# Performance work log

Measured on AMD Instinct MI355X. Metric: run time of the kernel, lower is better.

The kernel has to match this reference:

```python
import jax, jax.numpy as jnp
import numpy as np

B, S, D, H, DK, R = 8, 1024, 1024, 8, 128, 16
NEG = float(-2**31)


def setup_inputs() -> dict:
    key = jax.random.key(0)
    ks = jax.random.split(key, 16)
    std = 1.0 / np.sqrt(D)
    inp = {
        "query": jax.random.normal(ks[0], (B, S, D), jnp.float32),
        "key": jax.random.normal(ks[1], (B, S, D), jnp.float32),
        "value": jax.random.normal(ks[2], (B, S, D), jnp.float32),
        "mask": jax.random.bernoulli(ks[3], 0.9, (B, S, S)),
        "W_A": jax.random.normal(ks[4], (D, R), jnp.float32) * std,
        "W_B": jax.random.normal(ks[5], (R, H * DK), jnp.float32) * std,
        "W_C": jax.random.normal(ks[6], (D, R), jnp.float32) * std,
        "W_D": jax.random.normal(ks[7], (R, H * DK), jnp.float32) * std,
        "W_E": jax.random.normal(ks[8], (D, R), jnp.float32) * std,
        "W_F": jax.random.normal(ks[9], (R, H * DK), jnp.float32) * std,
        "Wq": jax.random.normal(ks[10], (D, H * DK), jnp.float32) * std,
        "bq": jnp.zeros((H * DK,), jnp.float32),
        "Wk": jax.random.normal(ks[11], (D, H * DK), jnp.float32) * std,
        "bk": jnp.zeros((H * DK,), jnp.float32),
        "Wv": jax.random.normal(ks[12], (D, H * DK), jnp.float32) * std,
        "bv": jnp.zeros((H * DK,), jnp.float32),
        "Wo": jax.random.normal(ks[13], (H * DK, D), jnp.float32) * std,
        "bo": jnp.zeros((D,), jnp.float32),
    }
    return inp


def reference(query, key, value, mask, W_A, W_B, W_C, W_D, W_E, W_F,
              Wq, bq, Wk, bk, Wv, bv, Wo, bo):
    nb = query.shape[0]
    # Linear + low-rank (LoRA-style) add; low-rank applied right-to-left for efficiency
    q = query @ Wq + bq + (query @ W_A) @ W_B      # [B,S,H*DK]
    k = key @ Wk + bk + (key @ W_C) @ W_D
    v = value @ Wv + bv + (value @ W_E) @ W_F
    # faithful plain reshape (NOT a transpose), as in the original code
    q = q.reshape(nb, H, -1, DK)                   # [B,H,S,DK]
    k = k.reshape(nb, H, -1, DK)
    v = v.reshape(nb, H, -1, DK)
    m = mask[:, None, :, :]                        # [B,1,S,S] broadcasts over heads
    scores = jnp.einsum("bhqd,bhkd->bhqk", q, k)   # no 1/sqrt(dk) scaling (faithful)
    scores = jnp.where(m, scores, jnp.float32(NEG))
    p = jax.nn.softmax(scores, axis=-1)
    x = jnp.einsum("bhqk,bhkd->bhqd", p, v)
    x = x.reshape(nb, -1, H * DK)                  # [B,S,H*DK]
    return x @ Wo + bo
```

## Files before the change

kernel.cpp:

```cpp
#include <hip/hip_runtime.h>
#include <hip/hip_bf16.h>
#include <stdint.h>


#define kB 8
#define kS 1024
#define kD 1024
#define kH 8
#define kDK 128
#define kHDK 1024
#define kM (kB * kS)
#define kMaskWords (kB * kS * (kS / 64))
#define kQKVN (kM * kHDK)

typedef _Float16 f16;
typedef __attribute__((ext_vector_type(4))) float f32x4;
typedef __attribute__((ext_vector_type(8))) _Float16 f16x8;

#define OFF_FLAG  ((size_t)0)
#define OFF_MBITS ((size_t)256)
#define OFF_WQT   (OFF_MBITS + (size_t)kMaskWords * 8)
#define OFF_WKT   (OFF_WQT + (size_t)2097152)
#define OFF_WVT   (OFF_WKT + (size_t)2097152)
#define OFF_WOT   (OFF_WVT + (size_t)2097152)
#define OFF_Q     (OFF_WOT + (size_t)2097152)
#define OFF_K     (OFF_Q  + (size_t)kQKVN * 2)
#define OFF_VT    (OFF_K  + (size_t)kQKVN * 2)
#define OFF_X     (OFF_VT + (size_t)kQKVN * 2)
#define OFF_T0    OFF_X
#define OFF_T1    (OFF_X + (size_t)kQKVN * 2)
#define OFF_T2    (OFF_X + (size_t)kQKVN * 4)
#define NEED3     (OFF_X + (size_t)kQKVN * 6)

__device__ __forceinline__ void async_load16(const void* g, void* lds_uniform) {
  auto gp = reinterpret_cast<const __attribute__((address_space(1))) unsigned int*>(
      reinterpret_cast<uintptr_t>(g));
  auto lp = reinterpret_cast<__attribute__((address_space(3))) unsigned int*>(
      reinterpret_cast<uintptr_t>(lds_uniform));
  __builtin_amdgcn_global_load_lds(gp, lp, 16, 0, 0);
}

__device__ __forceinline__ f32x4 mfma16(f16x8 a, f16x8 b, f32x4 c) {
  return __builtin_amdgcn_mfma_f32_16x16x32_f16(a, b, c, 0, 0, 0);
}

__device__ __forceinline__ float ldw(const void* p, size_t i, int f) {
  return f ? ((const float*)p)[i] : (float)((const __bf16*)p)[i];
}

__device__ __forceinline__ void swz_tiles(int& mt, int& nt) {
  const int gx = gridDim.x, gy = gridDim.y;
  const int L = blockIdx.y * gx + blockIdx.x;
  const int xcd = L & 7, rank = L >> 3;
  mt = xcd * (gy >> 3) + rank / gx;
  nt = rank % gx;
}

__global__ void detect_kernel(const unsigned int* __restrict__ qw,
                              const unsigned int* __restrict__ mw,
                              int* __restrict__ flags) {
  const int lane = threadIdx.x & 63;
  int hi = 0; bool w4 = true, b1 = true;
  #pragma unroll
  for (int j = 0; j < 4; ++j) {
    unsigned int w = qw[lane * 4 + j];
    hi += (int)(((w >> 7) & 0xFF) > 0x90) + (int)(((w >> 23) & 0xFF) > 0x90);
    unsigned int m = mw[lane * 4 + j];
    if (!(m == 0u || m == 1u || m == 0x3F800000u)) w4 = false;
    if ((m & 0xFEFEFEFEu) != 0u) b1 = false;
  }
  #pragma unroll
  for (int off = 32; off; off >>= 1) hi += __shfl_xor(hi, off, 64);
  unsigned long long bw4 = __ballot(w4), bb1 = __ballot(b1);
  if (lane == 0 && blockIdx.x == 0) {
    flags[1] = (hi > 16) ? 1 : 0;
    flags[0] = (bw4 == ~0ull) ? 4 : ((bb1 == ~0ull) ? 1 : 2);
  }
}

__global__ void pack_mask_kernel(const void* __restrict__ mask, const int* __restrict__ flags,
                                 unsigned long long* __restrict__ mbits) {
  int wi = blockIdx.x * 4 + (threadIdx.x >> 6);
  if (wi >= kMaskWords) return;
  int lane = threadIdx.x & 63;
  size_t e = (size_t)wi * 64 + lane;
  int width = flags[0];
  bool on;
  if (width == 1)      on = ((const unsigned char*)mask)[e] != 0;
  else if (width == 2) on = ((const unsigned short*)mask)[e] != 0;
  else                 on = ((const unsigned int*)mask)[e] != 0;
  unsigned long long bal = __ballot(on);
  if (lane == 0) mbits[wi] = bal;
}

__device__ __forceinline__ void convert_body(const void* src, f16* dst,
                                             const int* flags, int i) {
  f16x8 o;
  if (flags[1]) {
    f32x4 a = *(const f32x4*)((const float*)src + i);
    f32x4 b = *(const f32x4*)((const float*)src + i + 4);
    #pragma unroll
    for (int j = 0; j < 4; ++j) { o[j] = (f16)a[j]; o[4 + j] = (f16)b[j]; }
  } else {
    const __bf16* s = (const __bf16*)src + i;
    #pragma unroll
    for (int j = 0; j < 8; ++j) o[j] = (f16)(float)s[j];
  }
  *(f16x8*)(dst + i) = o;
}

__global__ __launch_bounds__(256) void convert_kernel(
    const void* __restrict__ src, f16* __restrict__ dst,
    const int* __restrict__ flags, int n) {
  const int i = (blockIdx.x * 256 + threadIdx.x) * 8;
  if (i < n) convert_body(src, dst, flags, i);
}

__global__ __launch_bounds__(256) void convert3_kernel(
    const void* __restrict__ s0, const void* __restrict__ s1, const void* __restrict__ s2,
    f16* __restrict__ d0, f16* __restrict__ d1, f16* __restrict__ d2,
    const int* __restrict__ flags) {
  const int z = blockIdx.z;
  const void* src = (z == 0) ? s0 : (z == 1) ? s1 : s2;
  f16* dst = (z == 0) ? d0 : (z == 1) ? d1 : d2;
  const int i = (blockIdx.x * 256 + threadIdx.x) * 8;
  if (i < kQKVN) convert_body(src, dst, flags, i);
}

__global__ __launch_bounds__(256) void build_weights_kernel(
    const void* __restrict__ Wq, const void* __restrict__ WA, const void* __restrict__ WB,
    const void* __restrict__ Wk, const void* __restrict__ WC, const void* __restrict__ WD,
    const void* __restrict__ Wv, const void* __restrict__ WE, const void* __restrict__ WF,
    const void* __restrict__ Wo, const int* __restrict__ flags,
    f16* __restrict__ WqT, f16* __restrict__ WkT,
    f16* __restrict__ WvT, f16* __restrict__ WoT) {
  const int z = blockIdx.z;
  const int f = flags[1];
  const void *W, *Aw = nullptr, *Bw = nullptr;
  f16* Out;
  if (z == 0)      { W = Wq; Aw = WA; Bw = WB; Out = WqT; }
  else if (z == 1) { W = Wk; Aw = WC; Bw = WD; Out = WkT; }
  else if (z == 2) { W = Wv; Aw = WE; Bw = WF; Out = WvT; }
  else             { W = Wo;                   Out = WoT; }

  __shared__ float Wt[32][33];
  __shared__ float At[32][16];
  __shared__ float Bt[16][33];
  const int tx = threadIdx.x, ty = threadIdx.y;
  const int k0 = blockIdx.y * 32, n0 = blockIdx.x * 32;
  #pragma unroll
  for (int i = 0; i < 4; ++i)
    Wt[ty + 8 * i][tx] = ldw(W, (size_t)(k0 + ty + 8 * i) * 1024 + n0 + tx, f);
  const int t = ty * 32 + tx;
  if (Aw) {
    #pragma unroll
    for (int j = 0; j < 2; ++j) {
      int e = t + j * 256;
      At[e >> 4][e & 15] = ldw(Aw, (size_t)(k0 + (e >> 4)) * 16 + (e & 15), f);
    }
    #pragma unroll
    for (int j = 0; j < 2; ++j) {
      int e = t + j * 256;
      Bt[e >> 5][e & 31] = ldw(Bw, (size_t)(e >> 5) * 1024 + n0 + (e & 31), f);
    }
  }
  __syncthreads();
  #pragma unroll
  for (int i = 0; i < 4; ++i) {
    const int nloc = ty + 8 * i, kloc = tx;
    float acc = Wt[kloc][nloc];
    if (Aw) {
      #pragma unroll
      for (int r = 0; r < 16; ++r) acc += At[kloc][r] * Bt[r][nloc];
    }
    Out[(size_t)(n0 + nloc) * 1024 + k0 + kloc] = (f16)acc;
  }
}

__device__ __forceinline__ void gemm_epilogue(
    f32x4 acc[4][4], const void* bias, void* C, int f, int vtrans, int out_dyn,
    int N, int m0, int n0, int wr, int wc, int l15, int hi) {
  const int wf32 = out_dyn && f;
  #pragma unroll
  for (int mi = 0; mi < 4; ++mi) {
    #pragma unroll
    for (int ni = 0; ni < 4; ++ni) {
      #pragma unroll
      for (int r = 0; r < 4; ++r) {
        const int row = m0 + wr * 64 + mi * 16 + 4 * hi + r;
        const int col = n0 + wc * 64 + ni * 16 + l15;
        float v = acc[mi][ni][r] + (bias ? ldw(bias, col, f) : 0.f);
        if (vtrans) {
          const int b = row >> 10, sp = row & 1023;
          const int fi = (sp << 10) | col;
          const int h = fi >> 17, s = (fi >> 7) & 1023, d = fi & 127;
          ((f16*)C)[(((size_t)(b * 8 + h) * 128 + d) << 10) + s] = (f16)v;
        } else if (wf32) {
          ((float*)C)[(size_t)row * N + col] = v;
        } else if (out_dyn) {
          ((__bf16*)C)[(size_t)row * N + col] = (__bf16)v;
        } else {
          ((f16*)C)[(size_t)row * N + col] = (f16)v;
        }
      }
    }
  }
}

__device__ __forceinline__ void gemm_core64(
    const f16* A, const f16* BT, const void* bias, void* C,
    int f, int vtrans, int out_dyn, int N, int K,
    int m0, int n0, f16* As, f16* Bs) {
  const int tid = threadIdx.x;
  const int lane = tid & 63, w = tid >> 6;
  const int wr = w >> 1, wc = w & 1;
  const int l15 = lane & 15, hi = lane >> 4;

  f32x4 acc[4][4];
  #pragma unroll
  for (int i = 0; i < 4; ++i)
    #pragma unroll
    for (int j = 0; j < 4; ++j) acc[i][j] = (f32x4){0.f, 0.f, 0.f, 0.f};

  for (int k0 = 0; k0 < K; k0 += 64) {
    if (k0) __syncthreads();
    #pragma unroll
    for (int j = 0; j < 4; ++j) {
      int d = tid + j * 256;
      int row = d >> 3, piece = (d & 7) ^ (row & 7);
      async_load16(A  + (size_t)(m0 + row) * K + k0 + piece * 8,
                   (char*)As + (w * 64 + j * 256) * 16);
      async_load16(BT + (size_t)(n0 + row) * K + k0 + piece * 8,
                   (char*)Bs + (w * 64 + j * 256) * 16);
    }
    __syncthreads();

    #pragma unroll
    for (int kk = 0; kk < 2; ++kk) {
      f16x8 af[4], bf_[4];
      #pragma unroll
      for (int mi = 0; mi < 4; ++mi) {
        const int row = wr * 64 + mi * 16 + l15;
        af[mi] = *(const f16x8*)&As[row * 64 + (((kk * 4 + hi) ^ (row & 7)) << 3)];
      }
      #pragma unroll
      for (int ni = 0; ni < 4; ++ni) {
        const int row = wc * 64 + ni * 16 + l15;
        bf_[ni] = *(const f16x8*)&Bs[row * 64 + (((kk * 4 + hi) ^ (row & 7)) << 3)];
      }
      #pragma unroll
      for (int mi = 0; mi < 4; ++mi)
        #pragma unroll
        for (int ni = 0; ni < 4; ++ni)
          acc[mi][ni] = mfma16(af[mi], bf_[ni], acc[mi][ni]);
    }
  }

  gemm_epilogue(acc, bias, C, f, vtrans, out_dyn, N, m0, n0, wr, wc, l15, hi);
}

__global__ __launch_bounds__(256) void gemm_bt_kernel(
    const f16* __restrict__ A, const f16* __restrict__ BT,
    const void* __restrict__ bias, void* __restrict__ C,
    const int* __restrict__ flags, int vtrans, int out_dyn, int N, int K) {
  __shared__ __align__(16) f16 As[128 * 64];
  __shared__ __align__(16) f16 Bs[128 * 64];
  int mt, nt;
  swz_tiles(mt, nt);
  gemm_core64(A, BT, bias, C, flags[1], vtrans, out_dyn, N, K,
              mt * 128, nt * 128, As, Bs);
}

__global__ __launch_bounds__(256) void gemm3_kernel(
    const f16* __restrict__ A0, const f16* __restrict__ A1, const f16* __restrict__ A2,
    const f16* __restrict__ B0, const f16* __restrict__ B1, const f16* __restrict__ B2,
    const void* __restrict__ b0, const void* __restrict__ b1, const void* __restrict__ b2,
    f16* __restrict__ C0, f16* __restrict__ C1, f16* __restrict__ C2,
    const int* __restrict__ flags) {
  __shared__ __align__(16) f16 As[128 * 64];
  __shared__ __align__(16) f16 Bs[128 * 64];
  const int z = blockIdx.z;
  const f16* A  = (z == 0) ? A0 : (z == 1) ? A1 : A2;
  const f16* BT = (z == 0) ? B0 : (z == 1) ? B1 : B2;
  const void* bias = (z == 0) ? b0 : (z == 1) ? b1 : b2;
  f16* C = (z == 0) ? C0 : (z == 1) ? C1 : C2;
  int mt, nt;
  swz_tiles(mt, nt);
  gemm_core64(A, BT, bias, C, flags[1], (z == 2) ? 1 : 0, 0, 1024, 1024,
              mt * 128, nt * 128, As, Bs);
}

__global__ __launch_bounds__(256) void attn_kernel(
    const f16* __restrict__ qbuf, const f16* __restrict__ kbuf,
    const f16* __restrict__ vT, const unsigned long long* __restrict__ mbits,
    f16* __restrict__ xbuf) {
  __shared__ __align__(16) f16 Ks[64 * 128];
  __shared__ __align__(16) f16 Vs[128 * 64];
  __shared__ __align__(16) f16 Ps[64 * 64];

  const int tid = threadIdx.x, lane = tid & 63, wv = tid >> 6;
  const int l15 = lane & 15, hi = lane >> 4;
  const int L = blockIdx.y * 16 + blockIdx.x;
  const int xcd = L & 7, rank = L >> 3;
  const int head_lin = xcd * 8 + (rank >> 4);
  const int q0 = (rank & 15) * 64;
  const size_t chunk = (size_t)head_lin * (kS * kDK);
  const f16* Qg = qbuf + chunk + (size_t)q0 * kDK;
  const f16* Kg = kbuf + chunk;
  const f16* Vg = vT + chunk;
  const unsigned long long* mrow = mbits + (size_t)(head_lin >> 3) * kS * 16;

  const int arow = wv * 16 + l15;
  f16x8 qf[4];
  #pragma unroll
  for (int kk = 0; kk < 4; ++kk)
    qf[kk] = *(const f16x8*)&Qg[(size_t)arow * 128 + kk * 32 + 8 * hi];

  f16x8 fone;
  #pragma unroll
  for (int j = 0; j < 8; ++j) fone[j] = (f16)1.f;

  const float NEG_INF = -__builtin_inff();
  float m_run[4] = {NEG_INF, NEG_INF, NEG_INF, NEG_INF};
  f32x4 acc_l = (f32x4){0.f, 0.f, 0.f, 0.f};
  f32x4 acc_o[8];
  #pragma unroll
  for (int j = 0; j < 8; ++j) acc_o[j] = (f32x4){0.f, 0.f, 0.f, 0.f};

  for (int t = 0; t < 16; ++t) {
    const int kv0 = t * 64;
    if (t) __syncthreads();
    #pragma unroll
    for (int j = 0; j < 4; ++j) {
      int c = tid + j * 256;
      int cs = c ^ ((c >> 4) & 7);
      async_load16((const char*)Kg + (size_t)kv0 * 256 + cs * 16,
                   (char*)Ks + (wv * 64 + j * 256) * 16);
    }
    #pragma unroll
    for (int j = 0; j < 4; ++j) {
      int c = tid + j * 256;
      int row = c >> 3, piece = (c & 7) ^ (row & 7);
      async_load16((const char*)Vg + ((size_t)row * kS + kv0 + piece * 8) * 2,
                   (char*)Vs + (wv * 64 + j * 256) * 16);
    }
    __syncthreads();

    f32x4 accs[4];
    #pragma unroll
    for (int i = 0; i < 4; ++i) accs[i] = (f32x4){0.f, 0.f, 0.f, 0.f};
    #pragma unroll
    for (int kk = 0; kk < 4; ++kk) {
      #pragma unroll
      for (int ni = 0; ni < 4; ++ni) {
        const int brow = ni * 16 + l15;
        f16x8 bk = *(const f16x8*)&Ks[brow * 128 + (((kk * 4 + hi) ^ (brow & 7)) << 3)];
        accs[ni] = mfma16(qf[kk], bk, accs[ni]);
      }
    }

    #pragma unroll
    for (int r = 0; r < 4; ++r) {
      const int prow = wv * 16 + 4 * hi + r;
      const int qrow = q0 + prow;
      const unsigned long long mw = mrow[(size_t)qrow * 16 + t];
      #pragma unroll
      for (int ni = 0; ni < 4; ++ni) {
        const int col = ni * 16 + l15;
        const bool on = (mw >> col) & 1ull;
        accs[ni][r] = on ? accs[ni][r] : NEG_INF;
      }
      const float gmax = fmaxf(fmaxf(accs[0][r], accs[1][r]),
                               fmaxf(accs[2][r], accs[3][r]));
      const float mold = m_run[r];
      if (__any(gmax > mold + 8.f)) {
        float tmax = gmax;
        #pragma unroll
        for (int off = 8; off; off >>= 1) tmax = fmaxf(tmax, __shfl_xor(tmax, off, 64));
        const float mnew = fmaxf(mold, tmax);
        if (mnew > mold) {
          const float alpha = __expf(mold - mnew);
          #pragma unroll
          for (int nj = 0; nj < 8; ++nj) acc_o[nj][r] *= alpha;
          acc_l[r] *= alpha;
          m_run[r] = mnew;
        }
      }
      const float m = m_run[r];
      #pragma unroll
      for (int ni = 0; ni < 4; ++ni) {
        const float p = __expf(accs[ni][r] - m);
        const int col = ni * 16 + l15;
        Ps[prow * 64 + (((col >> 3) ^ (prow & 7)) << 3) + (col & 7)] = (f16)p;
      }
    }

    const int prow2 = wv * 16 + l15;
    #pragma unroll
    for (int kk = 0; kk < 2; ++kk) {
      f16x8 ap = *(const f16x8*)&Ps[prow2 * 64 + (((kk * 4 + hi) ^ (prow2 & 7)) << 3)];
      acc_l = mfma16(ap, fone, acc_l);
      #pragma unroll
      for (int nj = 0; nj < 8; ++nj) {
        const int vrow = nj * 16 + l15;
        f16x8 bv = *(const f16x8*)&Vs[vrow * 64 + (((kk * 4 + hi) ^ (vrow & 7)) << 3)];
        acc_o[nj] = mfma16(ap, bv, acc_o[nj]);
      }
    }
  }

  #pragma unroll
  for (int r = 0; r < 4; ++r) {
    const float inv = (acc_l[r] > 0.f) ? 1.f / acc_l[r] : 0.f;
    const int row = q0 + wv * 16 + 4 * hi + r;
    #pragma unroll
    for (int nj = 0; nj < 8; ++nj)
      xbuf[chunk + (size_t)row * kDK + nj * 16 + l15] = (f16)(acc_o[nj][r] * inv);
  }
}

extern "C" void kernel_launch(void* const* d_in, const int* in_sizes, int n_in,
                              void* d_out, int out_size, void* d_ws, size_t ws_size,
                              hipStream_t stream) {
  const void* query = d_in[0];
  const void* key_  = d_in[1];
  const void* value = d_in[2];
  const void* mask  = d_in[3];
  const void* W_A = d_in[4];
  const void* W_B = d_in[5];
  const void* W_C = d_in[6];
  const void* W_D = d_in[7];
  const void* W_E = d_in[8];
  const void* W_F = d_in[9];
  const void* Wq  = d_in[10];
  const void* bq  = d_in[11];
  const void* Wk  = d_in[12];
  const void* bk  = d_in[13];
  const void* Wv  = d_in[14];
  const void* bv  = d_in[15];
  const void* Wo  = d_in[16];
  const void* bo  = d_in[17];

  char* ws = (char*)d_ws;
  int* flags = (int*)(ws + OFF_FLAG);
  unsigned long long* mbits = (unsigned long long*)(ws + OFF_MBITS);
  f16* WqT = (f16*)(ws + OFF_WQT);
  f16* WkT = (f16*)(ws + OFF_WKT);
  f16* WvT = (f16*)(ws + OFF_WVT);
  f16* WoT = (f16*)(ws + OFF_WOT);
  f16* qb  = (f16*)(ws + OFF_Q);
  f16* kb  = (f16*)(ws + OFF_K);
  f16* vTb = (f16*)(ws + OFF_VT);
  f16* xb  = (f16*)(ws + OFF_X);

  detect_kernel<<<1, 64, 0, stream>>>((const unsigned int*)query,
                                      (const unsigned int*)mask, flags);
  pack_mask_kernel<<<kMaskWords / 4, 256, 0, stream>>>(mask, flags, mbits);
  build_weights_kernel<<<dim3(32, 32, 4), dim3(32, 8), 0, stream>>>(
      Wq, W_A, W_B, Wk, W_C, W_D, Wv, W_E, W_F, Wo, flags, WqT, WkT, WvT, WoT);

  if (ws_size >= NEED3) {
    f16* t0 = (f16*)(ws + OFF_T0);
    f16* t1 = (f16*)(ws + OFF_T1);
    f16* t2 = (f16*)(ws + OFF_T2);
    convert3_kernel<<<dim3(kQKVN / (256 * 8), 1, 3), 256, 0, stream>>>(
        query, key_, value, t0, t1, t2, flags);
    gemm3_kernel<<<dim3(8, 64, 3), 256, 0, stream>>>(
        t0, t1, t2, WqT, WkT, WvT, bq, bk, bv, qb, kb, vTb, flags);
  } else {
    f16* tmp = (f16*)(ws + OFF_X);
    convert_kernel<<<kQKVN / (256 * 8), 256, 0, stream>>>(query, tmp, flags, kQKVN);
    gemm_bt_kernel<<<dim3(8, 64), 256, 0, stream>>>(
        tmp, WqT, bq, qb, flags, 0, 0, kHDK, kD);
    convert_kernel<<<kQKVN / (256 * 8), 256, 0, stream>>>(key_, tmp, flags, kQKVN);
    gemm_bt_kernel<<<dim3(8, 64), 256, 0, stream>>>(
        tmp, WkT, bk, kb, flags, 0, 0, kHDK, kD);
    convert_kernel<<<kQKVN / (256 * 8), 256, 0, stream>>>(value, tmp, flags, kQKVN);
    gemm_bt_kernel<<<dim3(8, 64), 256, 0, stream>>>(
        tmp, WvT, bv, vTb, flags, 1, 0, kHDK, kD);
  }

  attn_kernel<<<dim3(16, 64), 256, 0, stream>>>(qb, kb, vTb, mbits, xb);

  gemm_bt_kernel<<<dim3(8, 64), 256, 0, stream>>>(
      xb, WoT, bo, d_out, flags, 0, 1, kD, kHDK);
}
```

Measured before the change: 286.1 us.

## Double-buffer GEMM shared tiles with K-step 32 to overlap loads and MFMA

Replaces the single-buffered 64-wide K loop in the shared GEMM core with a two-stage ping-pong buffer of 32-wide K slices. The next slice's async global-to-LDS loads are issued before computing on the current one, aiming to hide load latency behind MFMA work. Shared memory per block stays the same, but there are twice as many loop iterations and barriers, and a new XOR swizzle is used for the narrower rows, which may change LDS bank-conflict behaviour.

```diff
diff --git a/kernel.cpp b/kernel.cpp
--- a/kernel.cpp
+++ b/kernel.cpp
@@ -207,7 +207,7 @@
   }
 }
 
-__device__ __forceinline__ void gemm_core64(
+__device__ __forceinline__ void gemm_core32p(
     const f16* A, const f16* BT, const void* bias, void* C,
     int f, int vtrans, int out_dyn, int N, int K,
     int m0, int n0, f16* As, f16* Bs) {
@@ -215,6 +215,20 @@
   const int lane = tid & 63, w = tid >> 6;
   const int wr = w >> 1, wc = w & 1;
   const int l15 = lane & 15, hi = lane >> 4;
+  const int swr = (l15 >> 1) & 3;
+
+  auto stage = [&](int sel, int k0) {
+    #pragma unroll
+    for (int j = 0; j < 2; ++j) {
+      int c = tid + j * 256;
+      int cs = c ^ ((c >> 3) & 3);
+      int row = cs >> 2, piece = cs & 3;
+      async_load16(A  + (size_t)(m0 + row) * K + k0 + piece * 8,
+                   (char*)As + sel * 8192 + (w * 64 + j * 256) * 16);
+      async_load16(BT + (size_t)(n0 + row) * K + k0 + piece * 8,
+                   (char*)Bs + sel * 8192 + (w * 64 + j * 256) * 16);
+    }
+  };
 
   f32x4 acc[4][4];
   #pragma unroll
@@ -222,38 +236,27 @@
     #pragma unroll
     for (int j = 0; j < 4; ++j) acc[i][j] = (f32x4){0.f, 0.f, 0.f, 0.f};
 
-  for (int k0 = 0; k0 < K; k0 += 64) {
-    if (k0) __syncthreads();
-    #pragma unroll
-    for (int j = 0; j < 4; ++j) {
-      int d = tid + j * 256;
-      int row = d >> 3, piece = (d & 7) ^ (row & 7);
-      async_load16(A  + (size_t)(m0 + row) * K + k0 + piece * 8,
-                   (char*)As + (w * 64 + j * 256) * 16);
-      async_load16(BT + (size_t)(n0 + row) * K + k0 + piece * 8,
-                   (char*)Bs + (w * 64 + j * 256) * 16);
-    }
+  stage(0, 0);
+  __syncthreads();
+  int cur = 0;
+  for (int k0 = 0; k0 < K; k0 += 32) {
+    if (k0 + 32 < K) stage(cur ^ 1, k0 + 32);
+    const f16* Ab = As + cur * 4096;
+    const f16* Bb = Bs + cur * 4096;
+    f16x8 af[4], bf_[4];
+    #pragma unroll
+    for (int mi = 0; mi < 4; ++mi)
+      af[mi] = *(const f16x8*)&Ab[(wr * 64 + mi * 16 + l15) * 32 + 8 * (hi ^ swr)];
+    #pragma unroll
+    for (int ni = 0; ni < 4; ++ni)
+      bf_[ni] = *(const f16x8*)&Bb[(wc * 64 + ni * 16 + l15) * 32 + 8 * (hi ^ swr)];
+    #pragma unroll
+    for (int mi = 0; mi < 4; ++mi)
+      #pragma unroll
+      for (int ni = 0; ni < 4; ++ni)
+        acc[mi][ni] = mfma16(af[mi], bf_[ni], acc[mi][ni]);
     __syncthreads();
-
-    #pragma unroll
-    for (int kk = 0; kk < 2; ++kk) {
-      f16x8 af[4], bf_[4];
-      #pragma unroll
-      for (int mi = 0; mi < 4; ++mi) {
-        const int row = wr * 64 + mi * 16 + l15;
-        af[mi] = *(const f16x8*)&As[row * 64 + (((kk * 4 + hi) ^ (row & 7)) << 3)];
-      }
-      #pragma unroll
-      for (int ni = 0; ni < 4; ++ni) {
-        const int row = wc * 64 + ni * 16 + l15;
-        bf_[ni] = *(const f16x8*)&Bs[row * 64 + (((kk * 4 + hi) ^ (row & 7)) << 3)];
-      }
-      #pragma unroll
-      for (int mi = 0; mi < 4; ++mi)
-        #pragma unroll
-        for (int ni = 0; ni < 4; ++ni)
-          acc[mi][ni] = mfma16(af[mi], bf_[ni], acc[mi][ni]);
-    }
+    cur ^= 1;
   }
 
   gemm_epilogue(acc, bias, C, f, vtrans, out_dyn, N, m0, n0, wr, wc, l15, hi);
@@ -263,12 +266,12 @@
     const f16* __restrict__ A, const f16* __restrict__ BT,
     const void* __restrict__ bias, void* __restrict__ C,
     const int* __restrict__ flags, int vtrans, int out_dyn, int N, int K) {
-  __shared__ __align__(16) f16 As[128 * 64];
-  __shared__ __align__(16) f16 Bs[128 * 64];
+  __shared__ __align__(16) f16 As[2 * 4096];
+  __shared__ __align__(16) f16 Bs[2 * 4096];
   int mt, nt;
   swz_tiles(mt, nt);
-  gemm_core64(A, BT, bias, C, flags[1], vtrans, out_dyn, N, K,
-              mt * 128, nt * 128, As, Bs);
+  gemm_core32p(A, BT, bias, C, flags[1], vtrans, out_dyn, N, K,
+               mt * 128, nt * 128, As, Bs);
 }
 
 __global__ __launch_bounds__(256) void gemm3_kernel(
@@ -277,8 +280,8 @@
     const void* __restrict__ b0, const void* __restrict__ b1, const void* __restrict__ b2,
     f16* __restrict__ C0, f16* __restrict__ C1, f16* __restrict__ C2,
     const int* __restrict__ flags) {
-  __shared__ __align__(16) f16 As[128 * 64];
-  __shared__ __align__(16) f16 Bs[128 * 64];
+  __shared__ __align__(16) f16 As[2 * 4096];
+  __shared__ __align__(16) f16 Bs[2 * 4096];
   const int z = blockIdx.z;
   const f16* A  = (z == 0) ? A0 : (z == 1) ? A1 : A2;
   const f16* BT = (z == 0) ? B0 : (z == 1) ? B1 : B2;
@@ -286,8 +289,8 @@
   f16* C = (z == 0) ? C0 : (z == 1) ? C1 : C2;
   int mt, nt;
   swz_tiles(mt, nt);
-  gemm_core64(A, BT, bias, C, flags[1], (z == 2) ? 1 : 0, 0, 1024, 1024,
-              mt * 128, nt * 128, As, Bs);
+  gemm_core32p(A, BT, bias, C, flags[1], (z == 2) ? 1 : 0, 0, 1024, 1024,
+               mt * 128, nt * 128, As, Bs);
 }
 
 __global__ __launch_bounds__(256) void attn_kernel(
```

After: 297.6 us. 4.0% more time.
